# Performance work log

Measured on AMD Instinct MI355X. Metric: run time of the kernel, lower is better.

The kernel has to match this reference:

```python
import jax, jax.numpy as jnp
import numpy as np

VOCAB = 32000
HIDDEN = 1024
BATCH = 4
SEQ = 2048


def setup_inputs() -> dict:
    key = jax.random.key(0)
    k_ids, k_w, k_b = jax.random.split(key, 3)
    input_ids = jax.random.randint(k_ids, (BATCH, SEQ), 0, VOCAB, dtype=jnp.int64 if jax.config.jax_enable_x64 else jnp.int32)
    # torch nn.Linear(vocab, hidden): weight [hidden, vocab], bias [hidden]
    W = jax.random.normal(k_w, (HIDDEN, VOCAB), dtype=jnp.float32) * (1.0 / np.sqrt(VOCAB))
    b = jax.random.normal(k_b, (HIDDEN,), dtype=jnp.float32) * 0.02
    return {"input_ids": input_ids, "W": W, "b": b}


def reference(input_ids, W, b):
    # Faithful to the original: one-hot the ids then run the dense Linear.
    # E: [B, S, V] one-hot float, out = E @ W^T + b -> [B, S, H]
    E = jax.nn.one_hot(input_ids, VOCAB, dtype=jnp.float32)
    X = jnp.einsum("bsv,hv->bsh", E, W) + b
    return X
```

## Files before the change

kernel.cpp:

```cpp
#include <hip/hip_runtime.h>


#define VOCAB   32000
#define HIDDEN  1024
#define CBIN    256
#define NBIN    125
#define ROWS    64
#define NCH     (HIDDEN/ROWS)
#define CHUNK   2048
#define NCHK    4
#define MSZ     384
#define NTOK    8192

__device__ __forceinline__ float bf2f(unsigned short h) {
    return __uint_as_float((unsigned)h << 16);
}
__device__ __forceinline__ unsigned pack2(float a, float b) {
    unsigned ua = __float_as_uint(a) + 0x8000u;
    unsigned ub = __float_as_uint(b) + 0x8000u;
    return __builtin_amdgcn_perm(ub, ua, 0x07060302u);
}

__global__ __launch_bounds__(256, 4) void fused_onehot_kernel(
    const int* __restrict__ ids,
    const float* __restrict__ W,
    const float* __restrict__ b,
    float* __restrict__ out)
{
    const int bin = blockIdx.x;
    const int c0  = bin * CBIN;
    const int h0  = blockIdx.y * ROWS;
    const int t   = threadIdx.x;

    __shared__ unsigned short tile[ROWS * CBIN];
    __shared__ int m_s[MSZ];
    __shared__ int cnt_s[NCHK];

    if (t < NCHK) cnt_s[t] = 0;

    const int c4 = (t & 63) * 4;
    const int r0 = t >> 6;
    float4 wv[16];
    #pragma unroll
    for (int i = 0; i < 16; ++i) {
        const int r = r0 + 4 * i;
        wv[i] = *reinterpret_cast<const float4*>(
            &W[(size_t)(h0 + r) * VOCAB + c0 + c4]);
    }
    #pragma unroll
    for (int i = 0; i < 16; ++i) {
        const int r  = r0 + 4 * i;
        const int cs = (c4 + (r & ~3)) & 255;
        *reinterpret_cast<uint2*>(&tile[r * CBIN + cs]) =
            make_uint2(pack2(wv[i].x, wv[i].y), pack2(wv[i].z, wv[i].w));
    }
    __syncthreads();

    const int g  = t & 15;
    const int q  = t >> 4;
    const int r4 = g * 4;
    const float4 bv = *reinterpret_cast<const float4*>(&b[h0 + r4]);

    for (int c = 0; c < NCHK; ++c) {
        if (c) __syncthreads();

        {
            const int4* p = reinterpret_cast<const int4*>(ids + c * CHUNK) + t * 2;
            const int4 a = p[0], e = p[1];
            const int v[8] = {a.x, a.y, a.z, a.w, e.x, e.y, e.z, e.w};
            const int tb = c * CHUNK + t * 8;
            #pragma unroll
            for (int k = 0; k < 8; ++k) {
                const int d = v[k] - c0;
                if ((unsigned)d < CBIN) {
                    const int p2 = atomicAdd(&cnt_s[c], 1);
                    if (p2 < MSZ) {
                        m_s[p2] = ((tb + k) << 8) | d;
                    } else {
                        const int tok = tb + k;
                        for (int r = 0; r < ROWS; ++r) {
                            const int cs2 = (d + (r & ~3)) & 255;
                            out[(size_t)tok * HIDDEN + h0 + r] =
                                bf2f(tile[r * CBIN + cs2]) + b[h0 + r];
                        }
                    }
                }
            }
        }
        __syncthreads();

        const int cnt = min(cnt_s[c], MSZ);
        for (int j = q; j < cnt; j += 16) {
            const int m   = m_s[j];
            const int tok = m >> 8;
            const int d   = m & 255;
            const int cs  = (d + r4) & 255;
            float4 o;
            o.x = bf2f(tile[(r4 + 0) * CBIN + cs]) + bv.x;
            o.y = bf2f(tile[(r4 + 1) * CBIN + cs]) + bv.y;
            o.z = bf2f(tile[(r4 + 2) * CBIN + cs]) + bv.z;
            o.w = bf2f(tile[(r4 + 3) * CBIN + cs]) + bv.w;
            *reinterpret_cast<float4*>(&out[(size_t)tok * HIDDEN + h0 + r4]) = o;
        }
    }
}

__global__ __launch_bounds__(256) void fallback_kernel(
    const int* __restrict__ ids, const float* __restrict__ W,
    const float* __restrict__ b, float* __restrict__ out, int n_tokens)
{
    const int t = threadIdx.x;
    const int sub = t >> 6, lane = t & 63;
    const int token = blockIdx.x * 4 + sub;
    if (token >= n_tokens) return;
    const int id = ids[token];
    const float* Wcol = W + (size_t)id;
    float v[16];
    #pragma unroll
    for (int j = 0; j < 4; ++j) {
        const int h0 = j * 256 + lane * 4;
        #pragma unroll
        for (int k = 0; k < 4; ++k)
            v[j * 4 + k] = Wcol[(size_t)(h0 + k) * VOCAB];
    }
    float* orow = out + (size_t)token * HIDDEN;
    #pragma unroll
    for (int j = 0; j < 4; ++j) {
        const int h0 = j * 256 + lane * 4;
        const float4 bv = *reinterpret_cast<const float4*>(&b[h0]);
        float4 o;
        o.x = v[j*4+0] + bv.x; o.y = v[j*4+1] + bv.y;
        o.z = v[j*4+2] + bv.z; o.w = v[j*4+3] + bv.w;
        *reinterpret_cast<float4*>(&orow[h0]) = o;
    }
}

extern "C" void kernel_launch(void* const* d_in, const int* in_sizes, int n_in,
                              void* d_out, int out_size, void* d_ws, size_t ws_size,
                              hipStream_t stream)
{
    const int*   ids = (const int*)d_in[0];
    const float* W   = (const float*)d_in[1];
    const float* b   = (const float*)d_in[2];
    float*       out = (float*)d_out;

    const int n_tokens = in_sizes[0];

    if (n_tokens == NTOK) {
        fused_onehot_kernel<<<dim3(NBIN, NCH), dim3(256), 0, stream>>>(
            ids, W, b, out);
    } else {
        fallback_kernel<<<dim3((n_tokens + 3) / 4), dim3(256), 0, stream>>>(
            ids, W, b, out, n_tokens);
    }
}
```

Before: 35.76 us.

## Replace LDS atomic compaction with per-wave ballot compaction overlapped with W loads

Token-id filtering now uses wave ballots and popcount prefix sums into per-wave match lists instead of shared-memory atomicAdd on per-chunk counters. All four id chunks are scanned once while the W tile loads are in flight, which removes the three extra block barriers between chunk phases. Overflow is handled by a rare second scan that writes the spilled tokens directly. The cost is a larger shared match buffer and a scatter phase that walks four per-wave lists.

New measurement: 33.92 us. 5.1% less time.

```diff
diff --git a/kernel.cpp b/kernel.cpp
--- a/kernel.cpp
+++ b/kernel.cpp
@@ -7,9 +7,7 @@
 #define NBIN    125
 #define ROWS    64
 #define NCH     (HIDDEN/ROWS)
-#define CHUNK   2048
-#define NCHK    4
-#define MSZ     384
+#define WCAP    256
 #define NTOK    8192
 
 __device__ __forceinline__ float bf2f(unsigned short h) {
@@ -31,12 +29,13 @@
     const int c0  = bin * CBIN;
     const int h0  = blockIdx.y * ROWS;
     const int t   = threadIdx.x;
+    const int w   = t >> 6;
+    const int lane = t & 63;
 
     __shared__ unsigned short tile[ROWS * CBIN];
-    __shared__ int m_s[MSZ];
-    __shared__ int cnt_s[NCHK];
-
-    if (t < NCHK) cnt_s[t] = 0;
+    __shared__ int m_s[4 * WCAP];
+    __shared__ int wcnt_s[4];
+    __shared__ int ovf_s[4];
 
     const int c4 = (t & 63) * 4;
     const int r0 = t >> 6;
@@ -47,6 +46,33 @@
         wv[i] = *reinterpret_cast<const float4*>(
             &W[(size_t)(h0 + r) * VOCAB + c0 + c4]);
     }
+
+    if (lane == 0) { wcnt_s[w] = 0; ovf_s[w] = 0; }
+    const unsigned long long lt = (1ull << lane) - 1ull;
+    int wcnt = 0;
+    #pragma unroll
+    for (int sp = 0; sp < 4; ++sp) {
+        const int4* p = reinterpret_cast<const int4*>(ids + sp * 2048) + t * 2;
+        const int4 a = p[0], e = p[1];
+        const int v[8] = {a.x, a.y, a.z, a.w, e.x, e.y, e.z, e.w};
+        #pragma unroll
+        for (int k = 0; k < 8; ++k) {
+            const int d = v[k] - c0;
+            const bool hit = (unsigned)d < (unsigned)CBIN;
+            const unsigned long long mm = __ballot(hit);
+            if (hit) {
+                const int idx = wcnt + __popcll(mm & lt);
+                if (idx < WCAP)
+                    m_s[w * WCAP + idx] = ((sp * 2048 + t * 8 + k) << 8) | d;
+                else
+                    ovf_s[w] = 1;
+                (void)0;
+            }
+            wcnt += (int)__popcll(mm);
+        }
+    }
+    if (lane == 0) wcnt_s[w] = wcnt;
+
     #pragma unroll
     for (int i = 0; i < 16; ++i) {
         const int r  = r0 + 4 * i;
@@ -54,6 +80,7 @@
         *reinterpret_cast<uint2*>(&tile[r * CBIN + cs]) =
             make_uint2(pack2(wv[i].x, wv[i].y), pack2(wv[i].z, wv[i].w));
     }
+
     __syncthreads();
 
     const int g  = t & 15;
@@ -61,37 +88,11 @@
     const int r4 = g * 4;
     const float4 bv = *reinterpret_cast<const float4*>(&b[h0 + r4]);
 
-    for (int c = 0; c < NCHK; ++c) {
-        if (c) __syncthreads();
-
-        {
-            const int4* p = reinterpret_cast<const int4*>(ids + c * CHUNK) + t * 2;
-            const int4 a = p[0], e = p[1];
-            const int v[8] = {a.x, a.y, a.z, a.w, e.x, e.y, e.z, e.w};
-            const int tb = c * CHUNK + t * 8;
-            #pragma unroll
-            for (int k = 0; k < 8; ++k) {
-                const int d = v[k] - c0;
-                if ((unsigned)d < CBIN) {
-                    const int p2 = atomicAdd(&cnt_s[c], 1);
-                    if (p2 < MSZ) {
-                        m_s[p2] = ((tb + k) << 8) | d;
-                    } else {
-                        const int tok = tb + k;
-                        for (int r = 0; r < ROWS; ++r) {
-                            const int cs2 = (d + (r & ~3)) & 255;
-                            out[(size_t)tok * HIDDEN + h0 + r] =
-                                bf2f(tile[r * CBIN + cs2]) + b[h0 + r];
-                        }
-                    }
-                }
-            }
-        }
-        __syncthreads();
-
-        const int cnt = min(cnt_s[c], MSZ);
+    #pragma unroll
+    for (int ws = 0; ws < 4; ++ws) {
+        const int cnt = min(wcnt_s[ws], WCAP);
         for (int j = q; j < cnt; j += 16) {
-            const int m   = m_s[j];
+            const int m   = m_s[ws * WCAP + j];
             const int tok = m >> 8;
             const int d   = m & 255;
             const int cs  = (d + r4) & 255;
@@ -101,6 +102,32 @@
             o.z = bf2f(tile[(r4 + 2) * CBIN + cs]) + bv.z;
             o.w = bf2f(tile[(r4 + 3) * CBIN + cs]) + bv.w;
             *reinterpret_cast<float4*>(&out[(size_t)tok * HIDDEN + h0 + r4]) = o;
+        }
+    }
+
+    if (ovf_s[w]) {
+        int rc = 0;
+        for (int sp = 0; sp < 4; ++sp) {
+            const int4* p = reinterpret_cast<const int4*>(ids + sp * 2048) + t * 2;
+            const int4 a = p[0], e = p[1];
+            const int v[8] = {a.x, a.y, a.z, a.w, e.x, e.y, e.z, e.w};
+            for (int k = 0; k < 8; ++k) {
+                const int d = v[k] - c0;
+                const bool hit = (unsigned)d < (unsigned)CBIN;
+                const unsigned long long mm = __ballot(hit);
+                if (hit) {
+                    const int idx = rc + __popcll(mm & lt);
+                    if (idx >= WCAP) {
+                        const int tok = sp * 2048 + t * 8 + k;
+                        for (int r = 0; r < ROWS; ++r) {
+                            const int cs2 = (d + (r & ~3)) & 255;
+                            out[(size_t)tok * HIDDEN + h0 + r] =
+                                bf2f(tile[r * CBIN + cs2]) + b[h0 + r];
+                        }
+                    }
+                }
+                rc += (int)__popcll(mm);
+            }
         }
     }
 }
```
